# Kernel optimization log

Hardware: AMD Instinct MI355X
Metric: run time of the kernel (lower is better)

The kernel has to match this reference:

```python
import jax, jax.numpy as jnp
import numpy as np

DIM = 1024
DEPTH = 4
HEADS = 16
DHEAD = 64
INNER = HEADS * DHEAD  # 1024
FF = 4 * DIM           # 4096
SCALE = DHEAD ** -0.5
LS_INIT = 0.1          # LayerScale init_eps for depth <= 18


def _layernorm(x, w, b):
    mu = jnp.mean(x, axis=-1, keepdims=True)
    var = jnp.mean((x - mu) ** 2, axis=-1, keepdims=True)
    return (x - mu) / jnp.sqrt(var + 1e-5) * w + b


def setup_inputs() -> dict:
    key = jax.random.key(0)
    ks = jax.random.split(key, 6)
    s = 0.02
    return {
        "x": jax.random.normal(ks[0], (2, 1024, DIM), dtype=jnp.float32),
        "ln1_w": jnp.ones((DEPTH, DIM), jnp.float32),
        "ln1_b": jnp.zeros((DEPTH, DIM), jnp.float32),
        "w_qkv": jax.random.normal(ks[1], (DEPTH, DIM, 3 * INNER), jnp.float32) * s,
        "w_out": jax.random.normal(ks[2], (DEPTH, INNER, DIM), jnp.float32) * s,
        "b_out": jnp.zeros((DEPTH, DIM), jnp.float32),
        "ls1": jnp.full((DEPTH, DIM), LS_INIT, jnp.float32),
        "ln2_w": jnp.ones((DEPTH, DIM), jnp.float32),
        "ln2_b": jnp.zeros((DEPTH, DIM), jnp.float32),
        "w_ff1": jax.random.normal(ks[3], (DEPTH, DIM, 2 * FF), jnp.float32) * s,
        "b_ff1": jnp.zeros((DEPTH, 2 * FF), jnp.float32),
        "w_ff2": jax.random.normal(ks[4], (DEPTH, FF, DIM), jnp.float32) * s,
        "b_ff2": jnp.zeros((DEPTH, DIM), jnp.float32),
        "ls2": jnp.full((DEPTH, DIM), LS_INIT, jnp.float32),
    }


def _block(x, p):
    (ln1w, ln1b, wqkv, wout, bout, ls1,
     ln2w, ln2b, wff1, bff1, wff2, bff2, ls2) = p
    b, n, _ = x.shape
    # --- PreNorm + Attention (non-causal, no mask) + LayerScale, residual ---
    h = _layernorm(x, ln1w, ln1b)
    qkv = h @ wqkv                                   # [b, n, 3*inner]
    q, k, v = jnp.split(qkv, 3, axis=-1)
    def heads(t):
        return t.reshape(b, n, HEADS, DHEAD).transpose(0, 2, 1, 3)  # b h n d
    q, k, v = heads(q) * SCALE, heads(k), heads(v)
    dots = jnp.einsum("bhid,bhjd->bhij", q, k)       # full O(n^2) scores
    attn = jax.nn.softmax(dots, axis=-1)
    o = jnp.einsum("bhij,bhjd->bhid", attn, v)
    o = o.transpose(0, 2, 1, 3).reshape(b, n, INNER)
    o = o @ wout + bout
    x = x + o * ls1
    # --- PreNorm + GEGLU FeedForward + LayerScale, residual ---
    h = _layernorm(x, ln2w, ln2b)
    u = h @ wff1 + bff1                              # [b, n, 2*FF]
    a, g = jnp.split(u, 2, axis=-1)
    ff = (a * jax.nn.gelu(g, approximate=False)) @ wff2 + bff2
    x = x + ff * ls2
    return x, None


def reference(x, ln1_w, ln1_b, w_qkv, w_out, b_out, ls1,
              ln2_w, ln2_b, w_ff1, b_ff1, w_ff2, b_ff2, ls2):
    ps = (ln1_w, ln1_b, w_qkv, w_out, b_out, ls1,
          ln2_w, ln2_b, w_ff1, b_ff1, w_ff2, b_ff2, ls2)
    out, _ = jax.lax.scan(_block, x, ps)
    return out
```

## Files before the change

kernel.cpp:

```cpp
#include <hip/hip_runtime.h>
#include <cstdint>
#include <cstddef>

typedef __bf16 bf16_t;
typedef __bf16 bf16x8 __attribute__((ext_vector_type(8)));
typedef __bf16 bf16x4 __attribute__((ext_vector_type(4)));
typedef float  f32x4  __attribute__((ext_vector_type(4)));

#define DEV __device__ __forceinline__

static constexpr int   BATCH = 2;
static constexpr int   NTOK  = 1024;
static constexpr int   DIM   = 1024;
static constexpr int   MROWS = BATCH * NTOK;
static constexpr float SCALE = 0.125f;

DEV void load_lds16(const bf16_t* g, bf16_t* s) {
  __builtin_amdgcn_global_load_lds(
      (const __attribute__((address_space(1))) void*)g,
      (__attribute__((address_space(3))) void*)s, 16, 0, 0);
}

DEV float wave_sum(float v) {
#pragma unroll
  for (int m = 1; m < 64; m <<= 1) v += __shfl_xor(v, m, 64);
  return v;
}
DEV float block_sum(float v, float* sb) {
  v = wave_sum(v);
  __syncthreads();
  if ((threadIdx.x & 63) == 0) sb[threadIdx.x >> 6] = v;
  __syncthreads();
  return sb[0] + sb[1] + sb[2] + sb[3];
}

template <int BM, int BN, int WR, int WC, int MODE>
__global__ __launch_bounds__(256) void gemm_bt(
    const bf16_t* __restrict__ A, long sA0, long sA1, int lda,
    const bf16_t* __restrict__ B, long sB0, long sB1, int ldb,
    void* __restrict__ Cv, long sC0, long sC1, int ldc,
    int K, float alpha, const float* __restrict__ bias,
    const float* __restrict__ ls) {
  constexpr int TM = BM / WR / 16;
  constexpr int TN = BN / WC / 16;
  __shared__ __attribute__((aligned(16))) bf16_t As[BM * 32];
  __shared__ __attribute__((aligned(16))) bf16_t Bs[BN * 32];

  const int tid  = threadIdx.x;
  const int lane = tid & 63, wave = tid >> 6;
  const int z  = blockIdx.z;
  const int zh = z >> 4, zl = z & 15;
  A += (size_t)zh * sA0 + (size_t)zl * sA1;
  B += (size_t)zh * sB0 + (size_t)zl * sB1;

  const int m0 = blockIdx.y * BM, n0 = blockIdx.x * BN;
  const int wm = (wave / WC) * (BM / WR);
  const int wn = (wave % WC) * (BN / WC);
  const int fm = lane & 15, quad = lane >> 4;

  f32x4 acc[TM][TN] = {};

  for (int k0 = 0; k0 < K; k0 += 32) {
#pragma unroll
    for (int c = tid; c < BM * 4; c += 256) {
      const int row = c >> 2, kc = (c & 3) << 3;
      load_lds16(A + (size_t)(m0 + row) * lda + k0 + kc, &As[c * 8]);
    }
#pragma unroll
    for (int c = tid; c < BN * 4; c += 256) {
      const int row = c >> 2, kc = (c & 3) << 3;
      load_lds16(B + (size_t)(n0 + row) * ldb + k0 + kc, &Bs[c * 8]);
    }
    __syncthreads();

    bf16x8 af[TM], bfr[TN];
#pragma unroll
    for (int i = 0; i < TM; ++i)
      af[i] = *(const bf16x8*)&As[(wm + i * 16 + fm) * 32 + quad * 8];
#pragma unroll
    for (int j = 0; j < TN; ++j)
      bfr[j] = *(const bf16x8*)&Bs[(wn + j * 16 + fm) * 32 + quad * 8];
#pragma unroll
    for (int i = 0; i < TM; ++i)
#pragma unroll
      for (int j = 0; j < TN; ++j)
        acc[i][j] = __builtin_amdgcn_mfma_f32_16x16x32_bf16(af[i], bfr[j],
                                                            acc[i][j], 0, 0, 0);
    __syncthreads();
  }

  const size_t coff = (size_t)zh * sC0 + (size_t)zl * sC1;
#pragma unroll
  for (int i = 0; i < TM; ++i) {
#pragma unroll
    for (int j = 0; j < TN; ++j) {
      const int col  = n0 + wn + j * 16 + fm;
      const int rowb = m0 + wm + i * 16 + quad * 4;
#pragma unroll
      for (int r = 0; r < 4; ++r) {
        const float  v   = acc[i][j][r];
        const size_t idx = coff + (size_t)(rowb + r) * ldc + col;
        if constexpr (MODE == 0) {
          ((bf16_t*)Cv)[idx] = (bf16_t)(v * alpha);
        } else if constexpr (MODE == 1) {
          ((bf16_t*)Cv)[idx] = (bf16_t)(v + bias[col]);
        } else {
          float* C = (float*)Cv;
          C[idx]   = C[idx] + (v + bias[col]) * ls[col];
        }
      }
    }
  }
}

__global__ __launch_bounds__(256) void flash_attn(
    const bf16_t* __restrict__ qkv,
    const bf16_t* __restrict__ vT,
    bf16_t* __restrict__ o) {
  constexpr int NT = 128;
  __shared__ __attribute__((aligned(16))) bf16_t Qs[2 * 64 * 32];
  __shared__ __attribute__((aligned(16))) bf16_t Ks[2 * NT * 32];
  __shared__ __attribute__((aligned(16))) bf16_t Vs[4 * 64 * 32];
  __shared__ __attribute__((aligned(16))) bf16_t Ps[4][4 * 16 * 32];

  const int tid = threadIdx.x, lane = tid & 63, wave = tid >> 6;
  const int fm = lane & 15, quad = lane >> 4;
  const int z = blockIdx.y, b = z >> 4, h = z & 15;
  const int q0 = blockIdx.x * 64;
  const bf16_t* qb  = qkv + (size_t)b * 1024 * 3072 + h * 64;
  const bf16_t* kb  = qb + 1024;
  const bf16_t* vtb = vT + (size_t)z * 64 * 1024;

  for (int c = tid; c < 512; c += 256) {
    const int kk = c >> 8, rr = (c >> 2) & 63, ii = c & 3;
    load_lds16(qb + (size_t)(q0 + rr) * 3072 + kk * 32 + ii * 8, &Qs[c * 8]);
  }
  __syncthreads();
  bf16x8 qf[2];
  qf[0] = *(const bf16x8*)&Qs[(wave * 16 + fm) * 32 + quad * 8];
  qf[1] = *(const bf16x8*)&Qs[64 * 32 + (wave * 16 + fm) * 32 + quad * 8];

  float mr[4], lr[4];
  f32x4 oacc[4];
#pragma unroll
  for (int r = 0; r < 4; ++r) { mr[r] = -1e30f; lr[r] = 0.f; }
#pragma unroll
  for (int t = 0; t < 4; ++t) oacc[t] = (f32x4){0.f, 0.f, 0.f, 0.f};

  for (int kv0 = 0; kv0 < 1024; kv0 += NT) {
    __syncthreads();
    for (int c = tid; c < NT * 8; c += 256) {
      const int kk = c >> 9, rr = (c >> 2) & 127, ii = c & 3;
      load_lds16(kb + (size_t)(kv0 + rr) * 3072 + kk * 32 + ii * 8, &Ks[c * 8]);
    }
    for (int c = tid; c < 1024; c += 256) {
      const int tc = c >> 8, rr = (c >> 2) & 63, ii = c & 3;
      load_lds16(vtb + (size_t)rr * 1024 + kv0 + tc * 32 + ii * 8, &Vs[c * 8]);
    }
    __syncthreads();

    f32x4 sc[8];
#pragma unroll
    for (int nt = 0; nt < 8; ++nt) {
      sc[nt] = (f32x4){0.f, 0.f, 0.f, 0.f};
#pragma unroll
      for (int kk = 0; kk < 2; ++kk) {
        const bf16x8 kf =
            *(const bf16x8*)&Ks[kk * NT * 32 + (nt * 16 + fm) * 32 + quad * 8];
        sc[nt] = __builtin_amdgcn_mfma_f32_16x16x32_bf16(qf[kk], kf, sc[nt],
                                                         0, 0, 0);
      }
    }
    float tmax[4] = {-1e30f, -1e30f, -1e30f, -1e30f};
#pragma unroll
    for (int nt = 0; nt < 8; ++nt)
#pragma unroll
      for (int r = 0; r < 4; ++r) {
        sc[nt][r] *= SCALE;
        tmax[r] = fmaxf(tmax[r], sc[nt][r]);
      }
#pragma unroll
    for (int m = 1; m < 16; m <<= 1)
#pragma unroll
      for (int r = 0; r < 4; ++r)
        tmax[r] = fmaxf(tmax[r], __shfl_xor(tmax[r], m, 64));
    float alpha[4], mn[4], ps[4];
#pragma unroll
    for (int r = 0; r < 4; ++r) {
      mn[r]    = fmaxf(mr[r], tmax[r]);
      alpha[r] = __expf(mr[r] - mn[r]);
      mr[r]    = mn[r];
      ps[r]    = 0.f;
    }
#pragma unroll
    for (int nt = 0; nt < 8; ++nt) {
      const int tcol = nt * 16 + fm, kk = tcol >> 5, tw = tcol & 31;
#pragma unroll
      for (int r = 0; r < 4; ++r) {
        const float p = __expf(sc[nt][r] - mn[r]);
        ps[r] += p;
        Ps[wave][kk * 512 + (quad * 4 + r) * 32 + tw] = (bf16_t)p;
      }
    }
#pragma unroll
    for (int m = 1; m < 16; m <<= 1)
#pragma unroll
      for (int r = 0; r < 4; ++r) ps[r] += __shfl_xor(ps[r], m, 64);
#pragma unroll
    for (int r = 0; r < 4; ++r) lr[r] = lr[r] * alpha[r] + ps[r];
#pragma unroll
    for (int t = 0; t < 4; ++t)
#pragma unroll
      for (int r = 0; r < 4; ++r) oacc[t][r] *= alpha[r];
    __builtin_amdgcn_s_waitcnt(0xC07F);
#pragma unroll
    for (int kk = 0; kk < 4; ++kk) {
      const bf16x8 af =
          *(const bf16x8*)&Ps[wave][kk * 512 + fm * 32 + quad * 8];
#pragma unroll
      for (int t = 0; t < 4; ++t) {
        const bf16x8 vf =
            *(const bf16x8*)&Vs[kk * 64 * 32 + (t * 16 + fm) * 32 + quad * 8];
        oacc[t] = __builtin_amdgcn_mfma_f32_16x16x32_bf16(af, vf, oacc[t],
                                                          0, 0, 0);
      }
    }
  }

  const size_t orow0 = (size_t)b * 1024 + q0 + wave * 16 + quad * 4;
#pragma unroll
  for (int t = 0; t < 4; ++t) {
    const int col = h * 64 + t * 16 + fm;
#pragma unroll
    for (int r = 0; r < 4; ++r)
      o[(orow0 + r) * 1024 + col] = (bf16_t)(oacc[t][r] / lr[r]);
  }
}

__global__ __launch_bounds__(256) void transpose_w(const float* __restrict__ W,
                                                   bf16_t* __restrict__ WT,
                                                   int K, int N) {
  __shared__ float t[32][33];
  const int n0 = blockIdx.x * 32, k0 = blockIdx.y * 32;
  const int tx = threadIdx.x & 31, ty = threadIdx.x >> 5;
#pragma unroll
  for (int s = 0; s < 4; ++s)
    t[ty + 8 * s][tx] = W[(size_t)(k0 + ty + 8 * s) * N + n0 + tx];
  __syncthreads();
#pragma unroll
  for (int s = 0; s < 4; ++s)
    WT[(size_t)(n0 + ty + 8 * s) * K + k0 + tx] = (bf16_t)t[tx][ty + 8 * s];
}

__global__ __launch_bounds__(256) void transpose_v(const bf16_t* __restrict__ qkv,
                                                   bf16_t* __restrict__ vT) {
  __shared__ bf16_t t[32][33];
  const int z = blockIdx.z, b = z >> 4, h = z & 15;
  const int d0 = blockIdx.y * 32, n0 = blockIdx.x * 32;
  const int tx = threadIdx.x & 31, ty = threadIdx.x >> 5;
  const bf16_t* src = qkv + (size_t)b * NTOK * 3072 + 2048 + h * 64;
#pragma unroll
  for (int s = 0; s < 4; ++s)
    t[ty + 8 * s][tx] = src[(size_t)(n0 + ty + 8 * s) * 3072 + d0 + tx];
  __syncthreads();
  bf16_t* dst = vT + (size_t)z * 64 * NTOK;
#pragma unroll
  for (int s = 0; s < 4; ++s)
    dst[(size_t)(d0 + ty + 8 * s) * NTOK + n0 + tx] = t[tx][ty + 8 * s];
}

__global__ __launch_bounds__(256) void ln_kernel(const float* __restrict__ x,
                                                 const float* __restrict__ w,
                                                 const float* __restrict__ b,
                                                 bf16_t* __restrict__ out) {
  __shared__ float sb[4];
  const int row = blockIdx.x, tid = threadIdx.x;
  const float4 v = ((const float4*)(x + (size_t)row * DIM))[tid];
  float s = v.x + v.y + v.z + v.w;
  s = block_sum(s, sb);
  const float mu = s * (1.f / DIM);
  const float dx = v.x - mu, dy = v.y - mu, dz = v.z - mu, dw = v.w - mu;
  float q = dx * dx + dy * dy + dz * dz + dw * dw;
  q = block_sum(q, sb);
  const float rstd = rsqrtf(q * (1.f / DIM) + 1e-5f);
  const float4 wv = ((const float4*)w)[tid];
  const float4 bv = ((const float4*)b)[tid];
  bf16x4 o;
  o[0] = (bf16_t)(dx * rstd * wv.x + bv.x);
  o[1] = (bf16_t)(dy * rstd * wv.y + bv.y);
  o[2] = (bf16_t)(dz * rstd * wv.z + bv.z);
  o[3] = (bf16_t)(dw * rstd * wv.w + bv.w);
  ((bf16x4*)(out + (size_t)row * DIM))[tid] = o;
}

__global__ __launch_bounds__(256) void geglu_kernel(const bf16_t* __restrict__ u,
                                                    bf16_t* __restrict__ ff) {
  const int g   = blockIdx.x * 256 + threadIdx.x;
  const int row = g >> 10, cg = (g & 1023) * 4;
  const bf16x4 av = *(const bf16x4*)(u + (size_t)row * 8192 + cg);
  const bf16x4 gv = *(const bf16x4*)(u + (size_t)row * 8192 + 4096 + cg);
  bf16x4 o;
#pragma unroll
  for (int c = 0; c < 4; ++c) {
    const float gx = (float)gv[c];
    const float ge = 0.5f * gx * (1.f + erff(gx * 0.70710678118654752f));
    o[c] = (bf16_t)((float)av[c] * ge);
  }
  *(bf16x4*)(ff + (size_t)row * 4096 + cg) = o;
}

extern "C" void kernel_launch(void* const* d_in, const int* in_sizes, int n_in,
                              void* d_out, int out_size, void* d_ws,
                              size_t ws_size, hipStream_t stream) {
  const float* x_in = (const float*)d_in[0];
  const float* ln1w = (const float*)d_in[1];
  const float* ln1b = (const float*)d_in[2];
  const float* wqkv = (const float*)d_in[3];
  const float* wout = (const float*)d_in[4];
  const float* bout = (const float*)d_in[5];
  const float* ls1  = (const float*)d_in[6];
  const float* ln2w = (const float*)d_in[7];
  const float* ln2b = (const float*)d_in[8];
  const float* wff1 = (const float*)d_in[9];
  const float* bff1 = (const float*)d_in[10];
  const float* wff2 = (const float*)d_in[11];
  const float* bff2 = (const float*)d_in[12];
  const float* ls2  = (const float*)d_in[13];
  float*       xout = (float*)d_out;

  char*   ws     = (char*)d_ws;
  bf16_t* wqkvT  = (bf16_t*)ws; ws += (size_t)3072 * 1024 * 2;
  bf16_t* woutT  = (bf16_t*)ws; ws += (size_t)1024 * 1024 * 2;
  bf16_t* wff1T  = (bf16_t*)ws; ws += (size_t)8192 * 1024 * 2;
  bf16_t* wff2T  = (bf16_t*)ws; ws += (size_t)1024 * 4096 * 2;
  bf16_t* h_bf   = (bf16_t*)ws; ws += (size_t)MROWS * 1024 * 2;
  bf16_t* qkv_bf = (bf16_t*)ws; ws += (size_t)MROWS * 3072 * 2;
  bf16_t* o_bf   = (bf16_t*)ws; ws += (size_t)MROWS * 1024 * 2;
  bf16_t* vT     = (bf16_t*)ws; ws += (size_t)32 * 64 * 1024 * 2;
  bf16_t* u_bf   = (bf16_t*)ws; ws += (size_t)MROWS * 8192 * 2;
  bf16_t* ff_bf  = (bf16_t*)ws; ws += (size_t)MROWS * 4096 * 2;
  if (ws_size < (size_t)(ws - (char*)d_ws)) return;

  hipMemcpyAsync(xout, x_in, (size_t)MROWS * DIM * 4,
                 hipMemcpyDeviceToDevice, stream);

  for (int l = 0; l < 4; ++l) {
    transpose_w<<<dim3(3072 / 32, 1024 / 32), 256, 0, stream>>>(
        wqkv + (size_t)l * 1024 * 3072, wqkvT, 1024, 3072);
    transpose_w<<<dim3(1024 / 32, 1024 / 32), 256, 0, stream>>>(
        wout + (size_t)l * 1024 * 1024, woutT, 1024, 1024);
    transpose_w<<<dim3(8192 / 32, 1024 / 32), 256, 0, stream>>>(
        wff1 + (size_t)l * 1024 * 8192, wff1T, 1024, 8192);
    transpose_w<<<dim3(1024 / 32, 4096 / 32), 256, 0, stream>>>(
        wff2 + (size_t)l * 4096 * 1024, wff2T, 4096, 1024);

    ln_kernel<<<MROWS, 256, 0, stream>>>(xout, ln1w + l * 1024,
                                         ln1b + l * 1024, h_bf);
    gemm_bt<128, 128, 2, 2, 0><<<dim3(24, 16, 1), 256, 0, stream>>>(
        h_bf, 0, 0, 1024, wqkvT, 0, 0, 1024, qkv_bf, 0, 0, 3072, 1024, 1.f,
        nullptr, nullptr);
    transpose_v<<<dim3(32, 2, 32), 256, 0, stream>>>(qkv_bf, vT);
    flash_attn<<<dim3(16, 32), 256, 0, stream>>>(qkv_bf, vT, o_bf);
    gemm_bt<64, 128, 1, 4, 2><<<dim3(8, 32, 1), 256, 0, stream>>>(
        o_bf, 0, 0, 1024, woutT, 0, 0, 1024, xout, 0, 0, 1024, 1024, 1.f,
        bout + l * 1024, ls1 + l * 1024);

    ln_kernel<<<MROWS, 256, 0, stream>>>(xout, ln2w + l * 1024,
                                         ln2b + l * 1024, h_bf);
    gemm_bt<128, 128, 2, 2, 1><<<dim3(64, 16, 1), 256, 0, stream>>>(
        h_bf, 0, 0, 1024, wff1T, 0, 0, 1024, u_bf, 0, 0, 8192, 1024, 1.f,
        bff1 + l * 8192, nullptr);
    geglu_kernel<<<8192, 256, 0, stream>>>(u_bf, ff_bf);
    gemm_bt<64, 128, 1, 4, 2><<<dim3(8, 32, 1), 256, 0, stream>>>(
        ff_bf, 0, 0, 4096, wff2T, 0, 0, 4096, xout, 0, 0, 1024, 4096, 1.f,
        bff2 + l * 1024, ls2 + l * 1024);
  }
}
```

Before: 1.226 ms.

## Fuse GEGLU and V-transpose into GEMM epilogues, merge weight transposes

The FF1 weight columns are interleaved during the transpose so each GEMM tile holds matching value and gate columns. GEGLU is then applied in the epilogue, which removes the u buffer round trip and the separate geglu kernel. The QKV GEMM writes V directly in transposed layout, dropping the transpose_v kernel but using strided scattered stores. The four weight transposes become one launch to reduce launch overhead.

Result: faster. 1.179 ms (-3.8%).

```diff
diff --git a/kernel.cpp b/kernel.cpp
--- a/kernel.cpp
+++ b/kernel.cpp
@@ -40,7 +40,7 @@
     const bf16_t* __restrict__ B, long sB0, long sB1, int ldb,
     void* __restrict__ Cv, long sC0, long sC1, int ldc,
     int K, float alpha, const float* __restrict__ bias,
-    const float* __restrict__ ls) {
+    const float* __restrict__ ls, bf16_t* __restrict__ vtp) {
   constexpr int TM = BM / WR / 16;
   constexpr int TN = BN / WC / 16;
   __shared__ __attribute__((aligned(16))) bf16_t As[BM * 32];
@@ -90,23 +90,66 @@
   }
 
   const size_t coff = (size_t)zh * sC0 + (size_t)zl * sC1;
-#pragma unroll
-  for (int i = 0; i < TM; ++i) {
-#pragma unroll
-    for (int j = 0; j < TN; ++j) {
-      const int col  = n0 + wn + j * 16 + fm;
+  if constexpr (MODE == 3) {
+    bf16_t* C = (bf16_t*)Cv;
+#pragma unroll
+    for (int i = 0; i < TM; ++i) {
       const int rowb = m0 + wm + i * 16 + quad * 4;
 #pragma unroll
-      for (int r = 0; r < 4; ++r) {
-        const float  v   = acc[i][j][r];
-        const size_t idx = coff + (size_t)(rowb + r) * ldc + col;
-        if constexpr (MODE == 0) {
-          ((bf16_t*)Cv)[idx] = (bf16_t)(v * alpha);
-        } else if constexpr (MODE == 1) {
-          ((bf16_t*)Cv)[idx] = (bf16_t)(v + bias[col]);
+      for (int p = 0; p < TN / 2; ++p) {
+        const int   cf = ((n0 + wn) >> 1) + p * 16 + fm;
+        const float ba = bias[cf], bg = bias[4096 + cf];
+#pragma unroll
+        for (int r = 0; r < 4; ++r) {
+          const float a  = acc[i][2 * p][r] + ba;
+          const float g  = acc[i][2 * p + 1][r] + bg;
+          const float ge = 0.5f * g * (1.f + erff(g * 0.70710678118654752f));
+          C[(size_t)(rowb + r) * ldc + cf] = (bf16_t)(a * ge);
+        }
+      }
+    }
+  } else if constexpr (MODE == 4) {
+    bf16_t* C = (bf16_t*)Cv;
+#pragma unroll
+    for (int i = 0; i < TM; ++i) {
+#pragma unroll
+      for (int j = 0; j < TN; ++j) {
+        const int col  = n0 + wn + j * 16 + fm;
+        const int rowb = m0 + wm + i * 16 + quad * 4;
+        if (col < 2048) {
+#pragma unroll
+          for (int r = 0; r < 4; ++r)
+            C[(size_t)(rowb + r) * ldc + col] = (bf16_t)acc[i][j][r];
         } else {
-          float* C = (float*)Cv;
-          C[idx]   = C[idx] + (v + bias[col]) * ls[col];
+          const int hh = (col - 2048) >> 6, d = (col - 2048) & 63;
+#pragma unroll
+          for (int r = 0; r < 4; ++r) {
+            const int row = rowb + r, bb = row >> 10, tok = row & 1023;
+            vtp[((size_t)(bb * 16 + hh) * 64 + d) * 1024 + tok] =
+                (bf16_t)acc[i][j][r];
+          }
+        }
+      }
+    }
+  } else {
+#pragma unroll
+    for (int i = 0; i < TM; ++i) {
+#pragma unroll
+      for (int j = 0; j < TN; ++j) {
+        const int col  = n0 + wn + j * 16 + fm;
+        const int rowb = m0 + wm + i * 16 + quad * 4;
+#pragma unroll
+        for (int r = 0; r < 4; ++r) {
+          const float  v   = acc[i][j][r];
+          const size_t idx = coff + (size_t)(rowb + r) * ldc + col;
+          if constexpr (MODE == 0) {
+            ((bf16_t*)Cv)[idx] = (bf16_t)(v * alpha);
+          } else if constexpr (MODE == 1) {
+            ((bf16_t*)Cv)[idx] = (bf16_t)(v + bias[col]);
+          } else {
+            float* C = (float*)Cv;
+            C[idx]   = C[idx] + (v + bias[col]) * ls[col];
+          }
         }
       }
     }
@@ -237,36 +280,48 @@
   }
 }
 
-__global__ __launch_bounds__(256) void transpose_w(const float* __restrict__ W,
-                                                   bf16_t* __restrict__ WT,
-                                                   int K, int N) {
+__global__ __launch_bounds__(256) void transpose_all(
+    const float* __restrict__ wqkv, const float* __restrict__ wout,
+    const float* __restrict__ wff1, const float* __restrict__ wff2,
+    bf16_t* __restrict__ wqkvT, bf16_t* __restrict__ woutT,
+    bf16_t* __restrict__ wff1T, bf16_t* __restrict__ wff2T, int l) {
   __shared__ float t[32][33];
-  const int n0 = blockIdx.x * 32, k0 = blockIdx.y * 32;
+  int bx = blockIdx.x;
+  const float* W;
+  bf16_t*      WT;
+  int N, K;
+  bool perm = false;
+  if (bx < 3072) {
+    W = wqkv + (size_t)l * 1024 * 3072; WT = wqkvT; K = 1024; N = 3072;
+  } else if (bx < 4096) {
+    bx -= 3072;
+    W = wout + (size_t)l * 1024 * 1024; WT = woutT; K = 1024; N = 1024;
+  } else if (bx < 12288) {
+    bx -= 4096;
+    W = wff1 + (size_t)l * 1024 * 8192; WT = wff1T; K = 1024; N = 8192;
+    perm = true;
+  } else {
+    bx -= 12288;
+    W = wff2 + (size_t)l * 4096 * 1024; WT = wff2T; K = 4096; N = 1024;
+  }
+  const int nbx = N >> 5;
+  const int n0 = (bx % nbx) * 32, k0 = (bx / nbx) * 32;
   const int tx = threadIdx.x & 31, ty = threadIdx.x >> 5;
 #pragma unroll
   for (int s = 0; s < 4; ++s)
     t[ty + 8 * s][tx] = W[(size_t)(k0 + ty + 8 * s) * N + n0 + tx];
   __syncthreads();
 #pragma unroll
-  for (int s = 0; s < 4; ++s)
-    WT[(size_t)(n0 + ty + 8 * s) * K + k0 + tx] = (bf16_t)t[tx][ty + 8 * s];
-}
-
-__global__ __launch_bounds__(256) void transpose_v(const bf16_t* __restrict__ qkv,
-                                                   bf16_t* __restrict__ vT) {
-  __shared__ bf16_t t[32][33];
-  const int z = blockIdx.z, b = z >> 4, h = z & 15;
-  const int d0 = blockIdx.y * 32, n0 = blockIdx.x * 32;
-  const int tx = threadIdx.x & 31, ty = threadIdx.x >> 5;
-  const bf16_t* src = qkv + (size_t)b * NTOK * 3072 + 2048 + h * 64;
-#pragma unroll
-  for (int s = 0; s < 4; ++s)
-    t[ty + 8 * s][tx] = src[(size_t)(n0 + ty + 8 * s) * 3072 + d0 + tx];
-  __syncthreads();
-  bf16_t* dst = vT + (size_t)z * 64 * NTOK;
-#pragma unroll
-  for (int s = 0; s < 4; ++s)
-    dst[(size_t)(d0 + ty + 8 * s) * NTOK + n0 + tx] = t[tx][ty + 8 * s];
+  for (int s = 0; s < 4; ++s) {
+    const int n = n0 + ty + 8 * s;
+    int r;
+    if (perm)
+      r = (n < 4096) ? (((n >> 4) << 5) + (n & 15))
+                     : ((((n - 4096) >> 4) << 5) + 16 + (n & 15));
+    else
+      r = n;
+    WT[(size_t)r * K + k0 + tx] = (bf16_t)t[tx][ty + 8 * s];
+  }
 }
 
 __global__ __launch_bounds__(256) void ln_kernel(const float* __restrict__ x,
@@ -293,22 +348,6 @@
   ((bf16x4*)(out + (size_t)row * DIM))[tid] = o;
 }
 
-__global__ __launch_bounds__(256) void geglu_kernel(const bf16_t* __restrict__ u,
-                                                    bf16_t* __restrict__ ff) {
-  const int g   = blockIdx.x * 256 + threadIdx.x;
-  const int row = g >> 10, cg = (g & 1023) * 4;
-  const bf16x4 av = *(const bf16x4*)(u + (size_t)row * 8192 + cg);
-  const bf16x4 gv = *(const bf16x4*)(u + (size_t)row * 8192 + 4096 + cg);
-  bf16x4 o;
-#pragma unroll
-  for (int c = 0; c < 4; ++c) {
-    const float gx = (float)gv[c];
-    const float ge = 0.5f * gx * (1.f + erff(gx * 0.70710678118654752f));
-    o[c] = (bf16_t)((float)av[c] * ge);
-  }
-  *(bf16x4*)(ff + (size_t)row * 4096 + cg) = o;
-}
-
 extern "C" void kernel_launch(void* const* d_in, const int* in_sizes, int n_in,
                               void* d_out, int out_size, void* d_ws,
                               size_t ws_size, hipStream_t stream) {
@@ -337,7 +376,6 @@
   bf16_t* qkv_bf = (bf16_t*)ws; ws += (size_t)MROWS * 3072 * 2;
   bf16_t* o_bf   = (bf16_t*)ws; ws += (size_t)MROWS * 1024 * 2;
   bf16_t* vT     = (bf16_t*)ws; ws += (size_t)32 * 64 * 1024 * 2;
-  bf16_t* u_bf   = (bf16_t*)ws; ws += (size_t)MROWS * 8192 * 2;
   bf16_t* ff_bf  = (bf16_t*)ws; ws += (size_t)MROWS * 4096 * 2;
   if (ws_size < (size_t)(ws - (char*)d_ws)) return;
 
@@ -345,34 +383,26 @@
                  hipMemcpyDeviceToDevice, stream);
 
   for (int l = 0; l < 4; ++l) {
-    transpose_w<<<dim3(3072 / 32, 1024 / 32), 256, 0, stream>>>(
-        wqkv + (size_t)l * 1024 * 3072, wqkvT, 1024, 3072);
-    transpose_w<<<dim3(1024 / 32, 1024 / 32), 256, 0, stream>>>(
-        wout + (size_t)l * 1024 * 1024, woutT, 1024, 1024);
-    transpose_w<<<dim3(8192 / 32, 1024 / 32), 256, 0, stream>>>(
-        wff1 + (size_t)l * 1024 * 8192, wff1T, 1024, 8192);
-    transpose_w<<<dim3(1024 / 32, 4096 / 32), 256, 0, stream>>>(
-        wff2 + (size_t)l * 4096 * 1024, wff2T, 4096, 1024);
+    transpose_all<<<dim3(16384), 256, 0, stream>>>(
+        wqkv, wout, wff1, wff2, wqkvT, woutT, wff1T, wff2T, l);
 
     ln_kernel<<<MROWS, 256, 0, stream>>>(xout, ln1w + l * 1024,
                                          ln1b + l * 1024, h_bf);
-    gemm_bt<128, 128, 2, 2, 0><<<dim3(24, 16, 1), 256, 0, stream>>>(
+    gemm_bt<128, 128, 2, 2, 4><<<dim3(24, 16, 1), 256, 0, stream>>>(
         h_bf, 0, 0, 1024, wqkvT, 0, 0, 1024, qkv_bf, 0, 0, 3072, 1024, 1.f,
-        nullptr, nullptr);
-    transpose_v<<<dim3(32, 2, 32), 256, 0, stream>>>(qkv_bf, vT);
+        nullptr, nullptr, vT);
     flash_attn<<<dim3(16, 32), 256, 0, stream>>>(qkv_bf, vT, o_bf);
     gemm_bt<64, 128, 1, 4, 2><<<dim3(8, 32, 1), 256, 0, stream>>>(
         o_bf, 0, 0, 1024, woutT, 0, 0, 1024, xout, 0, 0, 1024, 1024, 1.f,
-        bout + l * 1024, ls1 + l * 1024);
+        bout + l * 1024, ls1 + l * 1024, nullptr);
 
     ln_kernel<<<MROWS, 256, 0, stream>>>(xout, ln2w + l * 1024,
                                          ln2b + l * 1024, h_bf);
-    gemm_bt<128, 128, 2, 2, 1><<<dim3(64, 16, 1), 256, 0, stream>>>(
-        h_bf, 0, 0, 1024, wff1T, 0, 0, 1024, u_bf, 0, 0, 8192, 1024, 1.f,
-        bff1 + l * 8192, nullptr);
-    geglu_kernel<<<8192, 256, 0, stream>>>(u_bf, ff_bf);
+    gemm_bt<128, 128, 2, 2, 3><<<dim3(64, 16, 1), 256, 0, stream>>>(
+        h_bf, 0, 0, 1024, wff1T, 0, 0, 1024, ff_bf, 0, 0, 4096, 1024, 1.f,
+        bff1 + l * 8192, nullptr, nullptr);
     gemm_bt<64, 128, 1, 4, 2><<<dim3(8, 32, 1), 256, 0, stream>>>(
         ff_bf, 0, 0, 4096, wff2T, 0, 0, 4096, xout, 0, 0, 1024, 4096, 1.f,
-        bff2 + l * 1024, ls2 + l * 1024);
-  }
-}
+        bff2 + l * 1024, ls2 + l * 1024, nullptr);
+  }
+}
```
